# Optimization experiments

Measured on AMD Instinct MI355X. Metric: run time of the kernel, lower is better.

The kernel has to match this reference:

```python
import jax, jax.numpy as jnp
import numpy as np

B, D, L = 16, 64, 1280
H = 8            # nhead
WIN = 5          # window_size (divides L exactly)
DFF = 128        # dim_feedforward
EPS = 1e-5


def _layernorm(x, g, b):
    mu = jnp.mean(x, axis=-1, keepdims=True)
    var = jnp.mean(jnp.square(x - mu), axis=-1, keepdims=True)
    return (x - mu) * jax.lax.rsqrt(var + EPS) * g + b


def _mha(x, w_in, b_in, w_out, b_out):
    # x: (Bx, Lx, D). torch nn.MultiheadAttention, batch_first, eval mode.
    Bx, Lx, Dm = x.shape
    hd = Dm // H
    qkv = x @ w_in.T + b_in                      # (Bx, Lx, 3D)
    q, k, v = jnp.split(qkv, 3, axis=-1)
    q = q.reshape(Bx, Lx, H, hd)
    k = k.reshape(Bx, Lx, H, hd)
    v = v.reshape(Bx, Lx, H, hd)
    scale = 1.0 / jnp.sqrt(jnp.asarray(hd, x.dtype))
    scores = jnp.einsum('bqhd,bkhd->bhqk', q, k) * scale
    att = jax.nn.softmax(scores, axis=-1)
    out = jnp.einsum('bhqk,bkhd->bqhd', att, v).reshape(Bx, Lx, Dm)
    return out @ w_out.T + b_out


def setup_inputs() -> dict:
    key = jax.random.key(0)
    ks = jax.random.split(key, 16)
    s = 0.05
    return {
        'x': jax.random.normal(ks[0], (B, D, L), dtype=jnp.float32),
        # local attention params
        'lw_in': jax.random.normal(ks[1], (3 * D, D), dtype=jnp.float32) * s,
        'lb_in': jnp.zeros((3 * D,), jnp.float32),
        'lw_out': jax.random.normal(ks[2], (D, D), dtype=jnp.float32) * s,
        'lb_out': jnp.zeros((D,), jnp.float32),
        # global attention params
        'gw_in': jax.random.normal(ks[3], (3 * D, D), dtype=jnp.float32) * s,
        'gb_in': jnp.zeros((3 * D,), jnp.float32),
        'gw_out': jax.random.normal(ks[4], (D, D), dtype=jnp.float32) * s,
        'gb_out': jnp.zeros((D,), jnp.float32),
        # gating weight (init 0.5 like the module)
        'local_weight': jnp.full((D,), 0.5, jnp.float32),
        # layer norms
        'g1': jnp.ones((D,), jnp.float32), 'b1': jnp.zeros((D,), jnp.float32),
        'g2': jnp.ones((D,), jnp.float32), 'b2': jnp.zeros((D,), jnp.float32),
        'g3': jnp.ones((D,), jnp.float32), 'b3': jnp.zeros((D,), jnp.float32),
        # FFN
        'w1': jax.random.normal(ks[5], (DFF, D), dtype=jnp.float32) * s,
        'bf1': jnp.zeros((DFF,), jnp.float32),
        'w2': jax.random.normal(ks[6], (D, DFF), dtype=jnp.float32) * s,
        'bf2': jnp.zeros((D,), jnp.float32),
    }


def reference(x, lw_in, lb_in, lw_out, lb_out, gw_in, gb_in, gw_out, gb_out,
              local_weight, g1, b1, g2, b2, g3, b3, w1, bf1, w2, bf2):
    xt = jnp.transpose(x, (0, 2, 1))              # (B, L, D)
    residual = xt
    nW = L // WIN
    xw = xt.reshape(B * nW, WIN, D)
    local_out = _mha(xw, lw_in, lb_in, lw_out, lb_out).reshape(B, L, D)
    local_out = _layernorm(local_out + residual, g1, b1)
    # global attention
    global_out = _mha(xt, gw_in, gb_in, gw_out, gb_out)
    global_out = _layernorm(global_out + residual, g2, b2)
    # gated channel fusion
    alpha = jax.nn.sigmoid(local_weight)[None, None, :]
    fused = alpha * local_out + (1.0 - alpha) * global_out
    # FFN (dropout is identity in eval mode)
    ffn_out = jax.nn.relu(fused @ w1.T + bf1) @ w2.T + bf2
    out = _layernorm(ffn_out + fused, g3, b3)
    return jnp.transpose(out, (0, 2, 1))          # (B, D, L)
```

## Files before the change

kernel.cpp:

```cpp
#include <hip/hip_runtime.h>
#include <math.h>

typedef short bf16x8 __attribute__((ext_vector_type(8)));
typedef float f32x4 __attribute__((ext_vector_type(4)));
typedef float f32x16 __attribute__((ext_vector_type(16)));
typedef unsigned short u16;
typedef unsigned int u32;

#define RFL(x) __builtin_amdgcn_readfirstlane(x)

static __device__ __forceinline__ float bf2f(u16 s) {
  union { u32 u; float f; } c; c.u = ((u32)s) << 16; return c.f;
}
static __device__ __forceinline__ u16 f2bf(float f) {
  union { float f; u32 u; } c; c.f = f;
  u32 u = c.u + 0x7fffu + ((c.u >> 16) & 1u);
  return (u16)(u >> 16);
}
static __device__ __forceinline__ u32 pk2(float lo, float hi) {
  u32 r;
  asm("v_cvt_pk_bf16_f32 %0, %1, %2" : "=v"(r) : "v"(lo), "v"(hi));
  return r;
}
static __device__ __forceinline__ f32x4 MF(bf16x8 a, bf16x8 b, f32x4 c) {
  return __builtin_amdgcn_mfma_f32_16x16x32_bf16(a, b, c, 0, 0, 0);
}
static __device__ __forceinline__ f32x16 MF32(bf16x8 a, bf16x8 b, f32x16 c) {
  return __builtin_amdgcn_mfma_f32_32x32x16_bf16(a, b, c, 0, 0, 0);
}


__global__ __launch_bounds__(256) void qkvx(
    const float* __restrict__ x, const float* __restrict__ lw_in,
    const float* __restrict__ gw_in, const float* __restrict__ lb_in,
    const float* __restrict__ gb_in, u16* __restrict__ QKV) {
  __shared__ __align__(16) float xs[32][68];
  __shared__ __align__(16) u16 XTs[32 * 64];
  const int t = threadIdx.x;
  const int b = blockIdx.x / 40, l0 = (blockIdx.x % 40) * 32;
  for (int i = t; i < 2048; i += 256) {
    const int d = i >> 5, tok = i & 31;
    xs[tok][d] = x[(b * 64 + d) * 1280 + l0 + tok];
  }
  __syncthreads();
  {
    const int tok = t >> 3, c8 = (t & 7) * 8;
    union { bf16x8 v; u32 u[4]; } o;
    const float* src = &xs[tok][c8];
    o.u[0] = pk2(src[0], src[1]); o.u[1] = pk2(src[2], src[3]);
    o.u[2] = pk2(src[4], src[5]); o.u[3] = pk2(src[6], src[7]);
    const int byteoff = (tok * 128 + c8 * 2) ^ ((tok & 7) << 4);
    *(bf16x8*)((char*)XTs + byteoff) = o.v;
  }
  __syncthreads();
  const int lane = t & 63, w = RFL(t >> 6);
  const int lr = lane & 15, lg = lane >> 4;
  const int n0 = w * 96;
  bf16x8 a[2][2];
#pragma unroll
  for (int mt = 0; mt < 2; ++mt)
#pragma unroll
    for (int ks = 0; ks < 2; ++ks) {
      const int row = mt * 16 + lr;
      const int abyte = (row * 128 + ks * 64 + lg * 16) ^ ((row & 7) << 4);
      a[mt][ks] = *(const bf16x8*)((char*)XTs + abyte);
    }
  const float* W32 = (n0 < 192) ? lw_in : gw_in;
  const int nb = (n0 < 192) ? n0 : n0 - 192;
  bf16x8 bb[6][2];
#pragma unroll
  for (int nt = 0; nt < 6; ++nt)
#pragma unroll
    for (int ks = 0; ks < 2; ++ks) {
      const float* src = W32 + (nb + nt * 16 + lr) * 64 + ks * 32 + lg * 8;
      const float4 f0 = *(const float4*)src;
      const float4 f1 = *(const float4*)(src + 4);
      union { bf16x8 v; u32 u[4]; } o;
      o.u[0] = pk2(f0.x, f0.y); o.u[1] = pk2(f0.z, f0.w);
      o.u[2] = pk2(f1.x, f1.y); o.u[3] = pk2(f1.z, f1.w);
      bb[nt][ks] = o.v;
    }
  f32x4 acc[2][6];
#pragma unroll
  for (int mt = 0; mt < 2; ++mt)
#pragma unroll
    for (int nt = 0; nt < 6; ++nt) {
      f32x4 z = {0.f, 0.f, 0.f, 0.f};
      acc[mt][nt] = z;
#pragma unroll
      for (int ks = 0; ks < 2; ++ks)
        acc[mt][nt] = MF(a[mt][ks], bb[nt][ks], acc[mt][nt]);
    }
#pragma unroll
  for (int nt = 0; nt < 6; ++nt) {
    const int col = n0 + nt * 16 + lr;
    const float bias = (col < 192) ? lb_in[col] : gb_in[col - 192];
    const float scale = (col < 64) ? 0.35355339059327373f
                      : ((col >= 192 && col < 256) ? 65.29332172878775f : 1.f);
#pragma unroll
    for (int mt = 0; mt < 2; ++mt)
#pragma unroll
      for (int r = 0; r < 4; ++r) {
        const int row = b * 1280 + l0 + mt * 16 + 4 * lg + r;
        QKV[row * 384 + col] = f2bf((acc[mt][nt][r] + bias) * scale);
      }
  }
}

__global__ __launch_bounds__(256) void attn(
    const u16* __restrict__ QKV, u16* __restrict__ AOl,
    float* __restrict__ OSUM, float* __restrict__ OACC8,
    const float* __restrict__ lw_out, const float* __restrict__ gw_out,
    const float* __restrict__ w1, const float* __restrict__ w2,
    u16* __restrict__ Wlout, u16* __restrict__ Wgout,
    u16* __restrict__ W1b, u16* __restrict__ W2b) {
  __shared__ __align__(16) u16 Klds[640 * 8];
  __shared__ __align__(16) u16 VT[9 * 664];
  const int t = threadIdx.x;
  if (blockIdx.x < 20) {
    const int bh = blockIdx.y;
    const int b = bh >> 3, h = bh & 7;
    const int split = blockIdx.x & 1, qblk = blockIdx.x >> 1;
    const int k0 = split * 640;
    for (int l = t; l < 640; l += 256) {
      const int src = (b * 1280 + k0 + l) * 384 + h * 8;
      bf16x8 kv = *(const bf16x8*)(QKV + src + 256);
      bf16x8 vv = *(const bf16x8*)(QKV + src + 320);
      const int k5 = l & 31;
      const int pos = (l & ~31) +
                      ((k5 & 0x13) | ((k5 & 4) << 1) | ((k5 & 8) >> 1));
      *(bf16x8*)(Klds + pos * 8) = kv;
#pragma unroll
      for (int d = 0; d < 8; ++d) VT[d * 664 + l] = (u16)vv[d];
    }
    for (int l = t; l < 664; l += 256) VT[8 * 664 + l] = 0x3F80;
    __syncthreads();
    const int lane = t & 63, w = RFL(t >> 6);
    const int c = lane & 31, hi = lane >> 5;
    const int q = qblk * 128 + w * 32 + c;
    const bf16x8 qv = *(const bf16x8*)(QKV + (b * 1280 + q) * 384 + 192 + h * 8);
    const bf16x8 qz = {0, 0, 0, 0, 0, 0, 0, 0};
    const bf16x8 qf = (hi == 0) ? qv : qz;
    const u16* kp = Klds + c * 8;
    const int vrow = (c < 8) ? c : 8;
    const u16* vp = VT + vrow * 664 + hi * 8;
    f32x16 oaccA, oaccB, cmagic;
    const float CM = 12582912.0f + 16250.3f;
#pragma unroll
    for (int i = 0; i < 16; ++i) { oaccA[i] = 0.f; oaccB[i] = 0.f; cmagic[i] = CM; }
    auto step = [&](f32x16& oacc) {
      bf16x8 kf = *(const bf16x8*)kp;
      f32x16 s = MF32(kf, qf, cmagic);
      union { f32x16 f; u32 b[16]; } sb; sb.f = s;
      union { u32 u[4]; bf16x8 v; } pb1, pb2;
      pb1.u[0] = __builtin_amdgcn_perm(sb.b[1], sb.b[0], 0x05040100);
      pb1.u[1] = __builtin_amdgcn_perm(sb.b[3], sb.b[2], 0x05040100);
      pb1.u[2] = __builtin_amdgcn_perm(sb.b[5], sb.b[4], 0x05040100);
      pb1.u[3] = __builtin_amdgcn_perm(sb.b[7], sb.b[6], 0x05040100);
      pb2.u[0] = __builtin_amdgcn_perm(sb.b[9], sb.b[8], 0x05040100);
      pb2.u[1] = __builtin_amdgcn_perm(sb.b[11], sb.b[10], 0x05040100);
      pb2.u[2] = __builtin_amdgcn_perm(sb.b[13], sb.b[12], 0x05040100);
      pb2.u[3] = __builtin_amdgcn_perm(sb.b[15], sb.b[14], 0x05040100);
      bf16x8 vf1 = *(const bf16x8*)vp;
      oacc = MF32(vf1, pb1.v, oacc);
      bf16x8 vf2 = *(const bf16x8*)(vp + 16);
      oacc = MF32(vf2, pb2.v, oacc);
      kp += 256; vp += 32;
    };
#pragma unroll 2
    for (int jt2 = 0; jt2 < 10; ++jt2) {
      step(oaccA);
      step(oaccB);
    }
    f32x16 oacc;
#pragma unroll
    for (int i = 0; i < 16; ++i) oacc[i] = oaccA[i] + oaccB[i];
    const int qi = bh * 1280 + q;
    if (hi == 0) OSUM[split * 163840 + qi] = oacc[4];
    f32x4 od = {oacc[0], oacc[1], oacc[2], oacc[3]};
    *(f32x4*)(OACC8 + split * 1310720 + qi * 8 + hi * 4) = od;
    return;
  }
  const int lid = (blockIdx.x - 20) * 128 + blockIdx.y;
  if (lid < 640) {
    const int g = lid * 256 + t;
    const int qi = g % 5, h = (g / 5) & 7, wi = (g / 40) & 255, b = g / 10240;
    const int row = b * 1280 + wi * 5 + qi;
    float q[8];
    {
      bf16x8 qv = *(const bf16x8*)(QKV + row * 384 + h * 8);
#pragma unroll
      for (int d = 0; d < 8; ++d) q[d] = bf2f((u16)qv[d]);
    }
    float p[5], sum = 0.f;
#pragma unroll
    for (int j = 0; j < 5; ++j) {
      const int krow = b * 1280 + wi * 5 + j;
      bf16x8 kv = *(const bf16x8*)(QKV + krow * 384 + 64 + h * 8);
      float s = 0.f;
#pragma unroll
      for (int d = 0; d < 8; ++d) s = fmaf(q[d], bf2f((u16)kv[d]), s);
      p[j] = __expf(s); sum += p[j];
    }
    const float inv = 1.f / sum;
    float o[8] = {0, 0, 0, 0, 0, 0, 0, 0};
#pragma unroll
    for (int j = 0; j < 5; ++j) {
      const int vrow = b * 1280 + wi * 5 + j;
      bf16x8 vv = *(const bf16x8*)(QKV + vrow * 384 + 128 + h * 8);
#pragma unroll
      for (int d = 0; d < 8; ++d) o[d] = fmaf(p[j], bf2f((u16)vv[d]), o[d]);
    }
    union { bf16x8 v; u32 u[4]; } ov;
    ov.u[0] = pk2(o[0] * inv, o[1] * inv); ov.u[1] = pk2(o[2] * inv, o[3] * inv);
    ov.u[2] = pk2(o[4] * inv, o[5] * inv); ov.u[3] = pk2(o[6] * inv, o[7] * inv);
    *(bf16x8*)(AOl + row * 64 + h * 8) = ov.v;
  } else if (lid < 736) {
    const int f = (lid - 640) * 256 + t;
    if (f < 4096)       Wlout[f] = f2bf(lw_out[f]);
    else if (f < 8192)  Wgout[f - 4096] = f2bf(gw_out[f - 4096]);
    else if (f < 16384) W1b[f - 8192] = f2bf(w1[f - 8192]);
    else if (f < 24576) W2b[f - 16384] = f2bf(w2[f - 16384]);
  }
}

__global__ __launch_bounds__(64) void tail_kernel(
    const u16* __restrict__ AOl,
    const float* __restrict__ OSUM, const float* __restrict__ OACC8,
    const u16* __restrict__ Wlout, const u16* __restrict__ Wgout,
    const u16* __restrict__ W1b, const u16* __restrict__ W2b,
    const float* __restrict__ lb_out, const float* __restrict__ gb_out,
    const float* __restrict__ lwt,
    const float* __restrict__ g1, const float* __restrict__ b1,
    const float* __restrict__ g2, const float* __restrict__ b2,
    const float* __restrict__ g3, const float* __restrict__ b3,
    const float* __restrict__ bf1, const float* __restrict__ bf2,
    const float* __restrict__ x, float* __restrict__ out) {
  __shared__ __align__(16) float xso[64][20];
  __shared__ __align__(16) u16 Ft[16 * 64];
  __shared__ __align__(16) u16 Ht[16 * 128];
  const int t = threadIdx.x;
  const int b = blockIdx.y, l0 = blockIdx.x * 16;
  for (int i = t; i < 1024; i += 64) {
    const int d = i >> 4, tok = i & 15;
    xso[d][tok] = x[(b * 64 + d) * 1280 + l0 + tok];
  }
  __syncthreads();
  const int lr = t & 15, lg = (t & 63) >> 4;
  const int grow = b * 1280 + l0;

  f32x4 accl[4], accg[4];
#pragma unroll
  for (int nt = 0; nt < 4; ++nt) { f32x4 z = {0,0,0,0}; accl[nt] = z; accg[nt] = z; }
#pragma unroll
  for (int ks = 0; ks < 2; ++ks) {
    bf16x8 al = *(const bf16x8*)(AOl + (grow + lr) * 64 + ks * 32 + lg * 8);
    const int h = ks * 4 + lg;
    const int qi = (b * 8 + h) * 1280 + l0 + lr;
    f32x4 oa0 = *(const f32x4*)(OACC8 + qi * 8);
    f32x4 oa1 = *(const f32x4*)(OACC8 + qi * 8 + 4);
    f32x4 ob0 = *(const f32x4*)(OACC8 + 1310720 + qi * 8);
    f32x4 ob1 = *(const f32x4*)(OACC8 + 1310720 + qi * 8 + 4);
    const float inv = 1.f / (OSUM[qi] + OSUM[163840 + qi]);
    union { bf16x8 v; u32 u[4]; } agv;
    agv.u[0] = pk2((oa0[0] + ob0[0]) * inv, (oa0[1] + ob0[1]) * inv);
    agv.u[1] = pk2((oa0[2] + ob0[2]) * inv, (oa0[3] + ob0[3]) * inv);
    agv.u[2] = pk2((oa1[0] + ob1[0]) * inv, (oa1[1] + ob1[1]) * inv);
    agv.u[3] = pk2((oa1[2] + ob1[2]) * inv, (oa1[3] + ob1[3]) * inv);
#pragma unroll
    for (int nt = 0; nt < 4; ++nt) {
      bf16x8 bl = *(const bf16x8*)(Wlout + (nt * 16 + lr) * 64 + ks * 32 + lg * 8);
      bf16x8 bg = *(const bf16x8*)(Wgout + (nt * 16 + lr) * 64 + ks * 32 + lg * 8);
      accl[nt] = MF(al, bl, accl[nt]);
      accg[nt] = MF(agv.v, bg, accg[nt]);
    }
  }
#pragma unroll
  for (int nt = 0; nt < 4; ++nt) {
    const int col = nt * 16 + lr;
    const float bl = lb_out[col], bg = gb_out[col];
    f32x4 xr = *(const f32x4*)&xso[col][lg * 4];
#pragma unroll
    for (int r = 0; r < 4; ++r) {
      accl[nt][r] += bl + xr[r];
      accg[nt][r] += bg + xr[r];
    }
  }
  auto LN = [&](f32x4* a, const float* gam, const float* bet) {
    float gv[4], bv[4];
#pragma unroll
    for (int nt = 0; nt < 4; ++nt) { gv[nt] = gam[nt * 16 + lr]; bv[nt] = bet[nt * 16 + lr]; }
#pragma unroll
    for (int r = 0; r < 4; ++r) {
      float s = a[0][r] + a[1][r] + a[2][r] + a[3][r];
      s += __shfl_xor(s, 1); s += __shfl_xor(s, 2);
      s += __shfl_xor(s, 4); s += __shfl_xor(s, 8);
      const float mu = s * 0.015625f;
      float q = 0.f;
#pragma unroll
      for (int nt = 0; nt < 4; ++nt) { const float cv = a[nt][r] - mu; q = fmaf(cv, cv, q); }
      q += __shfl_xor(q, 1); q += __shfl_xor(q, 2);
      q += __shfl_xor(q, 4); q += __shfl_xor(q, 8);
      const float rsq = rsqrtf(q * 0.015625f + 1e-5f);
#pragma unroll
      for (int nt = 0; nt < 4; ++nt)
        a[nt][r] = (a[nt][r] - mu) * rsq * gv[nt] + bv[nt];
    }
  };
  LN(accl, g1, b1);
  LN(accg, g2, b2);
  f32x4 fus[4];
#pragma unroll
  for (int nt = 0; nt < 4; ++nt) {
    const int col = nt * 16 + lr;
    const float al_ = 1.f / (1.f + __expf(-lwt[col]));
#pragma unroll
    for (int r = 0; r < 4; ++r)
      fus[nt][r] = al_ * accl[nt][r] + (1.f - al_) * accg[nt][r];
  }
#pragma unroll
  for (int nt = 0; nt < 4; ++nt)
#pragma unroll
    for (int r = 0; r < 4; ++r) {
      const int ltok = lg * 4 + r;
      const int byteoff = (ltok * 128 + (nt * 16 + lr) * 2) ^ ((ltok & 7) << 4);
      *(u16*)((char*)Ft + byteoff) = f2bf(fus[nt][r]);
    }
  asm volatile("" ::: "memory");
  __syncthreads();
  f32x4 hcc[8];
#pragma unroll
  for (int nt = 0; nt < 8; ++nt) { f32x4 z = {0,0,0,0}; hcc[nt] = z; }
#pragma unroll
  for (int ks = 0; ks < 2; ++ks) {
    const int abyte = (lr * 128 + ks * 64 + lg * 16) ^ ((lr & 7) << 4);
    bf16x8 af = *(const bf16x8*)((char*)Ft + abyte);
#pragma unroll
    for (int nt = 0; nt < 8; ++nt) {
      bf16x8 bw = *(const bf16x8*)(W1b + (nt * 16 + lr) * 64 + ks * 32 + lg * 8);
      hcc[nt] = MF(af, bw, hcc[nt]);
    }
  }
#pragma unroll
  for (int nt = 0; nt < 8; ++nt) {
    const int f = nt * 16 + lr;
    const float bbv = bf1[f];
#pragma unroll
    for (int r = 0; r < 4; ++r) {
      const float v = fmaxf(hcc[nt][r] + bbv, 0.f);
      const int ltok = lg * 4 + r;
      const int byteoff = (ltok * 256 + f * 2) ^ ((ltok & 7) << 4);
      *(u16*)((char*)Ht + byteoff) = f2bf(v);
    }
  }
  asm volatile("" ::: "memory");
  f32x4 occ[4];
#pragma unroll
  for (int nt = 0; nt < 4; ++nt) { f32x4 z = {0,0,0,0}; occ[nt] = z; }
#pragma unroll
  for (int ks = 0; ks < 4; ++ks) {
    const int abyte = (lr * 256 + ks * 64 + lg * 16) ^ ((lr & 7) << 4);
    bf16x8 af = *(const bf16x8*)((char*)Ht + abyte);
#pragma unroll
    for (int nt = 0; nt < 4; ++nt) {
      bf16x8 bw = *(const bf16x8*)(W2b + (nt * 16 + lr) * 128 + ks * 32 + lg * 8);
      occ[nt] = MF(af, bw, occ[nt]);
    }
  }
#pragma unroll
  for (int nt = 0; nt < 4; ++nt) {
    const float bb2 = bf2[nt * 16 + lr];
#pragma unroll
    for (int r = 0; r < 4; ++r) occ[nt][r] += bb2 + fus[nt][r];
  }
  LN(occ, g3, b3);
#pragma unroll
  for (int nt = 0; nt < 4; ++nt)
#pragma unroll
    for (int r = 0; r < 4; ++r)
      xso[nt * 16 + lr][lg * 4 + r] = occ[nt][r];
  __syncthreads();
  for (int i = t; i < 1024; i += 64) {
    const int d = i >> 4, tok = i & 15;
    out[(b * 64 + d) * 1280 + l0 + tok] = xso[d][tok];
  }
}

extern "C" void kernel_launch(void* const* d_in, const int* in_sizes, int n_in,
                              void* d_out, int out_size, void* d_ws,
                              size_t ws_size, hipStream_t stream) {
  const float* x      = (const float*)d_in[0];
  const float* lw_in  = (const float*)d_in[1];
  const float* lb_in  = (const float*)d_in[2];
  const float* lw_out = (const float*)d_in[3];
  const float* lb_out = (const float*)d_in[4];
  const float* gw_in  = (const float*)d_in[5];
  const float* gb_in  = (const float*)d_in[6];
  const float* gw_out = (const float*)d_in[7];
  const float* gb_out = (const float*)d_in[8];
  const float* lwt    = (const float*)d_in[9];
  const float* g1 = (const float*)d_in[10]; const float* b1 = (const float*)d_in[11];
  const float* g2 = (const float*)d_in[12]; const float* b2 = (const float*)d_in[13];
  const float* g3 = (const float*)d_in[14]; const float* b3 = (const float*)d_in[15];
  const float* w1 = (const float*)d_in[16]; const float* bf1 = (const float*)d_in[17];
  const float* w2 = (const float*)d_in[18]; const float* bf2 = (const float*)d_in[19];
  float* out = (float*)d_out;

  u16* QKV   = (u16*)d_ws;
  u16* AOl   = QKV + 7864320;
  u16* Wlout = AOl + 1310720;
  u16* Wgout = Wlout + 4096;
  u16* W1b   = Wgout + 4096;
  u16* W2b   = W1b + 8192;
  float* OSUM  = (float*)(W2b + 8192);
  float* OACC8 = OSUM + 327680;

  qkvx<<<dim3(640), dim3(256), 0, stream>>>(x, lw_in, gw_in, lb_in, gb_in, QKV);
  attn<<<dim3(26, 128), dim3(256), 0, stream>>>(QKV, AOl, OSUM, OACC8,
                                                lw_out, gw_out, w1, w2,
                                                Wlout, Wgout, W1b, W2b);
  tail_kernel<<<dim3(80, 16), dim3(64), 0, stream>>>(
      AOl, OSUM, OACC8, Wlout, Wgout, W1b, W2b, lb_out, gb_out, lwt,
      g1, b1, g2, b2, g3, b3, bf1, bf2, x, out);
}
```

Before: 67.29 us.

## Write global K and V in attention-ready per-head layouts from the QKV kernel

The QKV projection kernel now writes the global K columns into a per-(batch,head) buffer with the row permutation the attention kernel expects. It writes the global V columns transposed per head and dimension. The attention kernel then fills its LDS with contiguous 16-byte copies, replacing strided gathers from the QKV buffer and scalar transposes of V into LDS. The cost is moved into the producer, which does scattered 2-byte writes for K and 8-byte writes for V, and the workspace grows by two buffers.

After: 65.00 us. 3.4% less time.

```diff
diff --git a/kernel.cpp b/kernel.cpp
--- a/kernel.cpp
+++ b/kernel.cpp
@@ -33,7 +33,8 @@
 __global__ __launch_bounds__(256) void qkvx(
     const float* __restrict__ x, const float* __restrict__ lw_in,
     const float* __restrict__ gw_in, const float* __restrict__ lb_in,
-    const float* __restrict__ gb_in, u16* __restrict__ QKV) {
+    const float* __restrict__ gb_in, u16* __restrict__ QKV,
+    u16* __restrict__ KTg, u16* __restrict__ VTg) {
   __shared__ __align__(16) float xs[32][68];
   __shared__ __align__(16) u16 XTs[32 * 64];
   const int t = threadIdx.x;
@@ -95,45 +96,68 @@
   for (int nt = 0; nt < 6; ++nt) {
     const int col = n0 + nt * 16 + lr;
     const float bias = (col < 192) ? lb_in[col] : gb_in[col - 192];
-    const float scale = (col < 64) ? 0.35355339059327373f
-                      : ((col >= 192 && col < 256) ? 65.29332172878775f : 1.f);
-#pragma unroll
-    for (int mt = 0; mt < 2; ++mt)
-#pragma unroll
-      for (int r = 0; r < 4; ++r) {
-        const int row = b * 1280 + l0 + mt * 16 + 4 * lg + r;
-        QKV[row * 384 + col] = f2bf((acc[mt][nt][r] + bias) * scale);
+    if (col < 256) {
+      const float scale = (col < 64) ? 0.35355339059327373f
+                        : ((col >= 192) ? 65.29332172878775f : 1.f);
+#pragma unroll
+      for (int mt = 0; mt < 2; ++mt)
+#pragma unroll
+        for (int r = 0; r < 4; ++r) {
+          const int row = b * 1280 + l0 + mt * 16 + 4 * lg + r;
+          QKV[row * 384 + col] = f2bf((acc[mt][nt][r] + bias) * scale);
+        }
+    } else if (col < 320) {
+      const int h = (col - 256) >> 3, d = (col - 256) & 7;
+      const int lgp = ((lg & 1) << 1) | (lg >> 1);
+#pragma unroll
+      for (int mt = 0; mt < 2; ++mt)
+#pragma unroll
+        for (int r = 0; r < 4; ++r) {
+          const int prow = l0 + mt * 16 + 4 * lgp + r;
+          KTg[((b * 8 + h) * 1280 + prow) * 8 + d] =
+              f2bf(acc[mt][nt][r] + bias);
+        }
+    } else {
+      const int h = (col - 320) >> 3, d = (col - 320) & 7;
+      const int rowbase = ((b * 8 + h) * 8 + d) * 1280;
+#pragma unroll
+      for (int mt = 0; mt < 2; ++mt) {
+        const int tok = l0 + mt * 16 + 4 * lg;
+        uint2 pv;
+        pv.x = pk2(acc[mt][nt][0] + bias, acc[mt][nt][1] + bias);
+        pv.y = pk2(acc[mt][nt][2] + bias, acc[mt][nt][3] + bias);
+        *(uint2*)(VTg + rowbase + tok) = pv;
       }
+    }
   }
 }
 
 __global__ __launch_bounds__(256) void attn(
-    const u16* __restrict__ QKV, u16* __restrict__ AOl,
+    const u16* __restrict__ QKV, const u16* __restrict__ KTg,
+    const u16* __restrict__ VTg, u16* __restrict__ AOl,
     float* __restrict__ OSUM, float* __restrict__ OACC8,
     const float* __restrict__ lw_out, const float* __restrict__ gw_out,
     const float* __restrict__ w1, const float* __restrict__ w2,
     u16* __restrict__ Wlout, u16* __restrict__ Wgout,
     u16* __restrict__ W1b, u16* __restrict__ W2b) {
   __shared__ __align__(16) u16 Klds[640 * 8];
-  __shared__ __align__(16) u16 VT[9 * 664];
+  __shared__ __align__(16) u16 VT[9 * 640];
   const int t = threadIdx.x;
   if (blockIdx.x < 20) {
     const int bh = blockIdx.y;
     const int b = bh >> 3, h = bh & 7;
     const int split = blockIdx.x & 1, qblk = blockIdx.x >> 1;
     const int k0 = split * 640;
-    for (int l = t; l < 640; l += 256) {
-      const int src = (b * 1280 + k0 + l) * 384 + h * 8;
-      bf16x8 kv = *(const bf16x8*)(QKV + src + 256);
-      bf16x8 vv = *(const bf16x8*)(QKV + src + 320);
-      const int k5 = l & 31;
-      const int pos = (l & ~31) +
-                      ((k5 & 0x13) | ((k5 & 4) << 1) | ((k5 & 8) >> 1));
-      *(bf16x8*)(Klds + pos * 8) = kv;
-#pragma unroll
-      for (int d = 0; d < 8; ++d) VT[d * 664 + l] = (u16)vv[d];
-    }
-    for (int l = t; l < 664; l += 256) VT[8 * 664 + l] = 0x3F80;
+    const uint4* Ksrc = (const uint4*)(KTg + (bh * 1280 + k0) * 8);
+    uint4* K4 = (uint4*)Klds;
+    for (int i = t; i < 640; i += 256) K4[i] = Ksrc[i];
+    const uint4* Vsrc = (const uint4*)(VTg + bh * 8 * 1280);
+    uint4* V4 = (uint4*)VT;
+    for (int i = t; i < 640; i += 256) {
+      const int d = i / 80, j = i % 80;
+      V4[d * 80 + j] = Vsrc[d * 160 + split * 80 + j];
+    }
+    for (int l = t; l < 640; l += 256) VT[8 * 640 + l] = 0x3F80;
     __syncthreads();
     const int lane = t & 63, w = RFL(t >> 6);
     const int c = lane & 31, hi = lane >> 5;
@@ -143,7 +167,7 @@
     const bf16x8 qf = (hi == 0) ? qv : qz;
     const u16* kp = Klds + c * 8;
     const int vrow = (c < 8) ? c : 8;
-    const u16* vp = VT + vrow * 664 + hi * 8;
+    const u16* vp = VT + vrow * 640 + hi * 8;
     f32x16 oaccA, oaccB, cmagic;
     const float CM = 12582912.0f + 16250.3f;
 #pragma unroll
@@ -408,16 +432,19 @@
 
   u16* QKV   = (u16*)d_ws;
   u16* AOl   = QKV + 7864320;
-  u16* Wlout = AOl + 1310720;
+  u16* KTg   = AOl + 1310720;
+  u16* VTg   = KTg + 1310720;
+  u16* Wlout = VTg + 1310720;
   u16* Wgout = Wlout + 4096;
   u16* W1b   = Wgout + 4096;
   u16* W2b   = W1b + 8192;
   float* OSUM  = (float*)(W2b + 8192);
   float* OACC8 = OSUM + 327680;
 
-  qkvx<<<dim3(640), dim3(256), 0, stream>>>(x, lw_in, gw_in, lb_in, gb_in, QKV);
-  attn<<<dim3(26, 128), dim3(256), 0, stream>>>(QKV, AOl, OSUM, OACC8,
-                                                lw_out, gw_out, w1, w2,
+  qkvx<<<dim3(640), dim3(256), 0, stream>>>(x, lw_in, gw_in, lb_in, gb_in,
+                                            QKV, KTg, VTg);
+  attn<<<dim3(26, 128), dim3(256), 0, stream>>>(QKV, KTg, VTg, AOl, OSUM,
+                                                OACC8, lw_out, gw_out, w1, w2,
                                                 Wlout, Wgout, W1b, W2b);
   tail_kernel<<<dim3(80, 16), dim3(64), 0, stream>>>(
       AOl, OSUM, OACC8, Wlout, Wgout, W1b, W2b, lb_out, gb_out, lwt,
```
